# Performance work log

Hardware: AMD Instinct MI355X
Metric: run time of the kernel (lower is better)

Reference implementation:

```python
import jax, jax.numpy as jnp
import numpy as np


def setup_inputs() -> dict:
    key = jax.random.key(0)
    k1, k2 = jax.random.split(key)
    B, A, H, W, C = 4, 9, 256, 256, 9
    F = 64
    lfi = jax.random.normal(k1, (B, A, H, W, C), dtype=jnp.float32)
    f_maps = jax.random.uniform(k2, (B, H, W, F), dtype=jnp.float32)
    return {"lfi": lfi, "f_maps": f_maps}


def reference(lfi, f_maps):
    # height mask: per (b, filter), mean of the [h,w] map over rows, normalized by its max.
    # f_maps: [B, H, W, F] -> hv: [B, W, F]; note original asserts W == H.
    hv = jnp.mean(f_maps, axis=1)                      # [B, W, F]
    hv = hv / jnp.max(hv, axis=1, keepdims=True)       # normalize per (b, f)
    h_mask = jnp.transpose(hv, (0, 2, 1))              # [B, F, H]
    # lfi: [B, A, H, W, C]; h_feat[b,f] = lfi[b] * h_mask[b,f,:] broadcast over H axis,
    # then mean over angular dims A and C -> factorizes as mean(lfi) * h_mask.
    m = jnp.mean(lfi, axis=(1, 4))                     # [B, H, W]
    out = jnp.einsum('bhw,bfh->bhwf', m, h_mask)       # [B, H, W, F]
    return out
```

## Files before the change

### kernel.cpp

```cpp
#include <hip/hip_runtime.h>

#define BB 4
#define AA 9
#define HH 256
#define WW 256
#define CC 9
#define FF 64

__global__ __launch_bounds__(256) void k_hv(const float* __restrict__ fm,
                                            float* __restrict__ hv) {
    const int blk = blockIdx.x;
    const int b = blk >> 8;
    const int w = blk & 255;
    const int f = threadIdx.x & 63;
    const int hl = threadIdx.x >> 6;

    const float* base = fm + (((size_t)b * HH) * WW + w) * FF + f;
    float s = 0.f;
#pragma unroll 8
    for (int h = hl; h < HH; h += 4) {
        s += base[(size_t)h * WW * FF];
    }
    __shared__ float sm[256];
    sm[threadIdx.x] = s;
    __syncthreads();
    if (hl == 0) {
        float t = sm[f] + sm[64 + f] + sm[128 + f] + sm[192 + f];
        hv[(size_t)blk * FF + f] = t * (1.0f / HH);
    }
}

__global__ __launch_bounds__(64) void k_inv(const float* __restrict__ hv,
                                            float* __restrict__ inv) {
    const int b = blockIdx.x >> 6;
    const int f = blockIdx.x & 63;
    const int t = threadIdx.x;
    float mx = -1e30f;
#pragma unroll
    for (int j = 0; j < 4; ++j) {
        mx = fmaxf(mx, hv[((size_t)b * WW + (t + 64 * j)) * FF + f]);
    }
#pragma unroll
    for (int off = 32; off; off >>= 1)
        mx = fmaxf(mx, __shfl_xor(mx, off));
    if (t == 0) inv[blockIdx.x] = 1.0f / mx;
}

__global__ __launch_bounds__(256) void k_m(const float* __restrict__ lfi,
                                           float* __restrict__ m) {
    const int t = threadIdx.x;
    const int k = blockIdx.x * 256 + t;
    const int b = k >> 16;
    const int blk_local = blockIdx.x & 255;
    const int r = t & 3;
    const size_t astride4 = (size_t)HH * WW * CC / 4;

    const float4* base = (const float4*)lfi + (size_t)b * AA * astride4 +
                         (size_t)blk_local * 576 + ((9 * t) >> 2);
    float acc = 0.f;
#pragma unroll 3
    for (int a = 0; a < AA; ++a) {
        const float4* p = base + (size_t)a * astride4;
        const float4 v0 = p[0], v1 = p[1], v2 = p[2];
        const float s12 = ((v0.x + v0.y) + (v0.z + v0.w)) +
                          ((v1.x + v1.y) + (v1.z + v1.w)) +
                          ((v2.x + v2.y) + (v2.z + v2.w));
        const float head = (r > 0 ? v0.x : 0.f) + (r > 1 ? v0.y : 0.f) +
                           (r > 2 ? v0.z : 0.f);
        const float tail = (r < 1 ? v2.y : 0.f) + (r < 2 ? v2.z : 0.f) +
                           (r < 3 ? v2.w : 0.f);
        acc += s12 - head - tail;
    }
    m[k] = acc * (1.0f / (AA * CC));
}

__global__ __launch_bounds__(256) void k_out(const float* __restrict__ m,
                                             const float* __restrict__ hv,
                                             const float* __restrict__ inv,
                                             float4* __restrict__ out) {
    const int idx = blockIdx.x * 256 + threadIdx.x;
    const int f4 = idx & 15;
    const int rest = idx >> 4;
    const int h = (rest >> 8) & 255;
    const int b = rest >> 16;

    const float mv = m[rest];
    const float4 hv4 = ((const float4*)hv)[((size_t)(b * HH + h)) * (FF / 4) + f4];
    const float4 iv4 = ((const float4*)inv)[b * (FF / 4) + f4];

    float4 o;
    o.x = mv * hv4.x * iv4.x;
    o.y = mv * hv4.y * iv4.y;
    o.z = mv * hv4.z * iv4.z;
    o.w = mv * hv4.w * iv4.w;
    out[idx] = o;
}

extern "C" void kernel_launch(void* const* d_in, const int* in_sizes, int n_in,
                              void* d_out, int out_size, void* d_ws, size_t ws_size,
                              hipStream_t stream) {
    const float* lfi = (const float*)d_in[0];
    const float* fm  = (const float*)d_in[1];
    float* out = (float*)d_out;

    char* ws = (char*)d_ws;
    float* hv  = (float*)ws;
    float* inv = (float*)(ws + (size_t)BB * WW * FF * 4);
    float* m   = (float*)(ws + (size_t)BB * WW * FF * 4 + 1024);

    k_hv<<<BB * WW, 256, 0, stream>>>(fm, hv);
    k_inv<<<BB * FF, 64, 0, stream>>>(hv, inv);
    k_m<<<(BB * HH * WW) / 256, 256, 0, stream>>>(lfi, m);
    k_out<<<(BB * HH * WW * FF / 4) / 256, 256, 0, stream>>>(m, hv, inv,
                                                             (float4*)out);
}
```

Before: 44.43 us.

## Fuse max-normalize, angular mean, and output broadcast into one kernel

Replaces the k_inv, k_m and k_out kernels with a single k_mout kernel, one block per (b,h) row. Each block recomputes the per-filter max over hv, computes the 256 angular means for its row into LDS, and writes the 64-wide output for the row. This removes two launches and the global round trip of the m and inv intermediates. In exchange every block redundantly rereads the full 64 KB hv slice for its batch to compute the max (1024 times in total), which should mostly hit in cache.

Result: slower. 49.07 us (+10.5%).

```diff
diff --git a/kernel.cpp b/kernel.cpp
--- a/kernel.cpp
+++ b/kernel.cpp
@@ -30,70 +30,68 @@
     }
 }
 
-__global__ __launch_bounds__(64) void k_inv(const float* __restrict__ hv,
-                                            float* __restrict__ inv) {
-    const int b = blockIdx.x >> 6;
-    const int f = blockIdx.x & 63;
+__global__ __launch_bounds__(256) void k_mout(const float* __restrict__ lfi,
+                                              const float* __restrict__ hv,
+                                              float4* __restrict__ out) {
     const int t = threadIdx.x;
-    float mx = -1e30f;
+    const int bh = blockIdx.x;
+    const int b = bh >> 8;
+    const int h = bh & 255;
+
+    __shared__ float sm_max[4][FF];
+    __shared__ float hvn_lds[FF];
+    __shared__ float m_lds[WW];
+
+    {
+        const int f = t & 63, q = t >> 6;
+        const float* hb = hv + (size_t)b * WW * FF + f;
+        float mx = -1e30f;
+#pragma unroll 8
+        for (int j = 0; j < 64; ++j)
+            mx = fmaxf(mx, hb[(size_t)(q * 64 + j) * FF]);
+        sm_max[q][f] = mx;
+    }
+
+    {
+        const int r = t & 3;
+        const size_t astride4 = (size_t)HH * WW * CC / 4;
+        const float4* base = (const float4*)lfi + (size_t)b * AA * astride4 +
+                             (size_t)h * 576 + ((9 * t) >> 2);
+        float acc = 0.f;
+#pragma unroll 3
+        for (int a = 0; a < AA; ++a) {
+            const float4* p = base + (size_t)a * astride4;
+            const float4 v0 = p[0], v1 = p[1], v2 = p[2];
+            const float s12 = ((v0.x + v0.y) + (v0.z + v0.w)) +
+                              ((v1.x + v1.y) + (v1.z + v1.w)) +
+                              ((v2.x + v2.y) + (v2.z + v2.w));
+            const float head = (r > 0 ? v0.x : 0.f) + (r > 1 ? v0.y : 0.f) +
+                               (r > 2 ? v0.z : 0.f);
+            const float tail = (r < 1 ? v2.y : 0.f) + (r < 2 ? v2.z : 0.f) +
+                               (r < 3 ? v2.w : 0.f);
+            acc += s12 - head - tail;
+        }
+        m_lds[t] = acc * (1.0f / (AA * CC));
+    }
+    __syncthreads();
+
+    if (t < FF) {
+        const float mx = fmaxf(fmaxf(sm_max[0][t], sm_max[1][t]),
+                               fmaxf(sm_max[2][t], sm_max[3][t]));
+        hvn_lds[t] = hv[(size_t)bh * FF + t] / mx;
+    }
+    __syncthreads();
+
+    const int f4 = t & 15;
+    const float4 hvn = ((const float4*)hvn_lds)[f4];
+    float4* ob = out + (size_t)bh * (WW * FF / 4);
 #pragma unroll
-    for (int j = 0; j < 4; ++j) {
-        mx = fmaxf(mx, hv[((size_t)b * WW + (t + 64 * j)) * FF + f]);
+    for (int k = 0; k < 16; ++k) {
+        const float mv = m_lds[k * 16 + (t >> 4)];
+        float4 o;
+        o.x = mv * hvn.x; o.y = mv * hvn.y; o.z = mv * hvn.z; o.w = mv * hvn.w;
+        ob[k * 256 + t] = o;
     }
-#pragma unroll
-    for (int off = 32; off; off >>= 1)
-        mx = fmaxf(mx, __shfl_xor(mx, off));
-    if (t == 0) inv[blockIdx.x] = 1.0f / mx;
-}
-
-__global__ __launch_bounds__(256) void k_m(const float* __restrict__ lfi,
-                                           float* __restrict__ m) {
-    const int t = threadIdx.x;
-    const int k = blockIdx.x * 256 + t;
-    const int b = k >> 16;
-    const int blk_local = blockIdx.x & 255;
-    const int r = t & 3;
-    const size_t astride4 = (size_t)HH * WW * CC / 4;
-
-    const float4* base = (const float4*)lfi + (size_t)b * AA * astride4 +
-                         (size_t)blk_local * 576 + ((9 * t) >> 2);
-    float acc = 0.f;
-#pragma unroll 3
-    for (int a = 0; a < AA; ++a) {
-        const float4* p = base + (size_t)a * astride4;
-        const float4 v0 = p[0], v1 = p[1], v2 = p[2];
-        const float s12 = ((v0.x + v0.y) + (v0.z + v0.w)) +
-                          ((v1.x + v1.y) + (v1.z + v1.w)) +
-                          ((v2.x + v2.y) + (v2.z + v2.w));
-        const float head = (r > 0 ? v0.x : 0.f) + (r > 1 ? v0.y : 0.f) +
-                           (r > 2 ? v0.z : 0.f);
-        const float tail = (r < 1 ? v2.y : 0.f) + (r < 2 ? v2.z : 0.f) +
-                           (r < 3 ? v2.w : 0.f);
-        acc += s12 - head - tail;
-    }
-    m[k] = acc * (1.0f / (AA * CC));
-}
-
-__global__ __launch_bounds__(256) void k_out(const float* __restrict__ m,
-                                             const float* __restrict__ hv,
-                                             const float* __restrict__ inv,
-                                             float4* __restrict__ out) {
-    const int idx = blockIdx.x * 256 + threadIdx.x;
-    const int f4 = idx & 15;
-    const int rest = idx >> 4;
-    const int h = (rest >> 8) & 255;
-    const int b = rest >> 16;
-
-    const float mv = m[rest];
-    const float4 hv4 = ((const float4*)hv)[((size_t)(b * HH + h)) * (FF / 4) + f4];
-    const float4 iv4 = ((const float4*)inv)[b * (FF / 4) + f4];
-
-    float4 o;
-    o.x = mv * hv4.x * iv4.x;
-    o.y = mv * hv4.y * iv4.y;
-    o.z = mv * hv4.z * iv4.z;
-    o.w = mv * hv4.w * iv4.w;
-    out[idx] = o;
 }
 
 extern "C" void kernel_launch(void* const* d_in, const int* in_sizes, int n_in,
@@ -103,14 +101,8 @@
     const float* fm  = (const float*)d_in[1];
     float* out = (float*)d_out;
 
-    char* ws = (char*)d_ws;
-    float* hv  = (float*)ws;
-    float* inv = (float*)(ws + (size_t)BB * WW * FF * 4);
-    float* m   = (float*)(ws + (size_t)BB * WW * FF * 4 + 1024);
+    float* hv = (float*)d_ws;
 
     k_hv<<<BB * WW, 256, 0, stream>>>(fm, hv);
-    k_inv<<<BB * FF, 64, 0, stream>>>(hv, inv);
-    k_m<<<(BB * HH * WW) / 256, 256, 0, stream>>>(lfi, m);
-    k_out<<<(BB * HH * WW * FF / 4) / 256, 256, 0, stream>>>(m, hv, inv,
-                                                             (float4*)out);
+    k_mout<<<BB * HH, 256, 0, stream>>>(lfi, hv, (float4*)out);
 }
```
